# Performance work log

Measured on AMD Instinct MI355X. Metric: run time of the kernel, lower is better.

## Reference

```python
import jax, jax.numpy as jnp
import numpy as np

DIM = 1024
NUM_HEADS = 16
HEAD_DIM = DIM // NUM_HEADS


def setup_inputs() -> dict:
    key = jax.random.key(0)
    ks = jax.random.split(key, 16)
    B, Sx, Sy = 4, 1024, 1024
    s = 1.0 / np.sqrt(DIM)
    inp = {
        'x': jax.random.normal(ks[0], (B, Sx, DIM), dtype=jnp.float32),
        'y': jax.random.normal(ks[1], (B, Sy, DIM), dtype=jnp.float32),
    }
    names = ['Kx', 'Qx', 'Vx', 'Ky', 'Vy', 'out']
    for i, n in enumerate(names):
        inp[f'W_{n}'] = jax.random.uniform(ks[2 + 2 * i], (DIM, DIM), dtype=jnp.float32, minval=-s, maxval=s)
        inp[f'b_{n}'] = jax.random.uniform(ks[3 + 2 * i], (DIM,), dtype=jnp.float32, minval=-s, maxval=s)
    return inp


def _heads(t, B, S):
    # [B, S, DIM] -> [B, H, S, Dh]
    return t.reshape(B, S, NUM_HEADS, HEAD_DIM).transpose(0, 2, 1, 3)


def _attn(x, y, W_Kx, b_Kx, W_Qx, b_Qx, W_Vx, b_Vx, W_Ky, b_Ky, W_Vy, b_Vy, W_out, b_out):
    B, Sx, _ = x.shape
    Sy = y.shape[1]
    lin = lambda t, W, b: t @ W.T + b
    Q = _heads(lin(x, W_Qx, b_Qx), B, Sx)
    Kc = jnp.concatenate([_heads(lin(x, W_Kx, b_Kx), B, Sx), _heads(lin(y, W_Ky, b_Ky), B, Sy)], axis=2)
    Vc = jnp.concatenate([_heads(lin(x, W_Vx, b_Vx), B, Sx), _heads(lin(y, W_Vy, b_Vy), B, Sy)], axis=2)
    scores = jnp.einsum('bhqd,bhkd->bhqk', Q, Kc) / np.sqrt(HEAD_DIM).astype(np.float32)
    w = jax.nn.softmax(scores, axis=-1)
    o = jnp.einsum('bhqk,bhkd->bhqd', w, Vc)  # [B, H, Sx, Dh]
    o = o.transpose(0, 2, 1, 3).reshape(B, Sx, DIM)
    return lin(o, W_out, b_out)


def reference(x, y, W_Kx, b_Kx, W_Qx, b_Qx, W_Vx, b_Vx, W_Ky, b_Ky, W_Vy, b_Vy, W_out, b_out):
    return _attn(x, y, W_Kx, b_Kx, W_Qx, b_Qx, W_Vx, b_Vx, W_Ky, b_Ky, W_Vy, b_Vy, W_out, b_out)
```

## Files before the change

kernel.cpp:

```cpp
#include <hip/hip_runtime.h>

#define DIMN 1024
#define NH 16
#define DH 64
#define SXX 1024
#define SKV 2048

typedef __bf16 bf16x8 __attribute__((ext_vector_type(8)));
typedef float f32x4 __attribute__((ext_vector_type(4)));
typedef unsigned short us8 __attribute__((ext_vector_type(8)));

__device__ __forceinline__ unsigned short f2bs(float f) {
    return (unsigned short)((__builtin_bit_cast(unsigned int, f) + 0x8000u) >> 16);
}
__device__ __forceinline__ unsigned int pk2(float a, float b) {
    return ((__builtin_bit_cast(unsigned int, a) + 0x8000u) >> 16)
         | ((__builtin_bit_cast(unsigned int, b) + 0x8000u) & 0xffff0000u);
}
__device__ __forceinline__ void gl_lds16(const void* g, void* l) {
    __builtin_amdgcn_global_load_lds(
        (const __attribute__((address_space(1))) unsigned int*)g,
        (__attribute__((address_space(3))) unsigned int*)l, 16, 0, 0);
}

struct CvtArgs {
    const float* src[8];
    unsigned short* dst[8];
    int start[8];
};
__global__ __launch_bounds__(256) void cvt_all(CvtArgs a) {
    int b = blockIdx.x;
    int r = 0;
#pragma unroll
    for (int i = 1; i < 8; i++) r += (b >= a.start[i]);
    int off = ((b - a.start[r]) * 256 + (int)threadIdx.x) * 8;
    const float* s = a.src[r] + off;
    float4 f0 = *(const float4*)(s);
    float4 f1 = *(const float4*)(s + 4);
    us8 o;
    o[0] = f2bs(f0.x); o[1] = f2bs(f0.y); o[2] = f2bs(f0.z); o[3] = f2bs(f0.w);
    o[4] = f2bs(f1.x); o[5] = f2bs(f1.y); o[6] = f2bs(f1.z); o[7] = f2bs(f1.w);
    *(us8*)(a.dst[r] + off) = o;
}

__device__ __forceinline__ void gemm_core(const unsigned short* __restrict__ A,
                                          const unsigned short* __restrict__ W,
                                          unsigned short* As, unsigned short* Bs,
                                          int m0, int n0, f32x4 (&acc)[4][4]) {
    const int K = DIMN;
    int tid = threadIdx.x, wave = tid >> 6, lane = tid & 63;
    int l15 = lane & 15, quad = lane >> 4;
    int wm = wave >> 1, wn = wave & 1;
    int srow = wave * 8 + (lane >> 3);
    int gcol = ((lane & 7) ^ (lane >> 3)) * 8;
    const unsigned short* gA = A + (size_t)(m0 + srow) * K + gcol;
    const unsigned short* gW = W + (size_t)(n0 + srow) * K + gcol;
    int ldsoff = wave * 512;
    int slot0 = (quad ^ (l15 & 7)) * 8;

    auto stage = [&](int buf, int k0) {
        unsigned short* lA = As + buf * 8192 + ldsoff;
        unsigned short* lB = Bs + buf * 8192 + ldsoff;
#pragma unroll
        for (int j = 0; j < 4; j++) {
            gl_lds16(gA + k0 + (size_t)j * 32 * K, lA + j * 2048);
            gl_lds16(gW + k0 + (size_t)j * 32 * K, lB + j * 2048);
        }
    };

    stage(0, 0);
    for (int k0 = 0; k0 < K; k0 += 64) {
        int buf = (k0 >> 6) & 1;
        __syncthreads();
        if (k0 + 64 < K) stage(buf ^ 1, k0 + 64);
        const unsigned short* as = As + buf * 8192;
        const unsigned short* bs = Bs + buf * 8192;
#pragma unroll
        for (int kk = 0; kk < 2; kk++) {
            int sl = slot0 ^ (kk * 32);
            bf16x8 af[4], bf[4];
#pragma unroll
            for (int mi = 0; mi < 4; mi++)
                af[mi] = __builtin_bit_cast(bf16x8, *(const us8*)(&as[(wm * 64 + mi * 16 + l15) * 64 + sl]));
#pragma unroll
            for (int ni = 0; ni < 4; ni++)
                bf[ni] = __builtin_bit_cast(bf16x8, *(const us8*)(&bs[(wn * 64 + ni * 16 + l15) * 64 + sl]));
#pragma unroll
            for (int mi = 0; mi < 4; mi++)
#pragma unroll
                for (int ni = 0; ni < 4; ni++)
                    acc[mi][ni] = __builtin_amdgcn_mfma_f32_16x16x32_bf16(af[mi], bf[ni], acc[mi][ni], 0, 0, 0);
        }
    }
}

__global__ __launch_bounds__(256, 2) void gemm_proj(
        const unsigned short* __restrict__ xb, const unsigned short* __restrict__ yb,
        const unsigned short* __restrict__ Wb,
        const float* __restrict__ b_Kx, const float* __restrict__ b_Qx, const float* __restrict__ b_Ky,
        const float* __restrict__ b_Vx, const float* __restrict__ b_Vy,
        unsigned short* __restrict__ Qd, unsigned short* __restrict__ Kd,
        unsigned short* __restrict__ Vd, float qscale) {
    __shared__ __align__(16) unsigned short As[2 * 128 * 64];
    __shared__ __align__(16) unsigned short Bs[2 * 128 * 64];
    int bx = blockIdx.x;
    int tid = threadIdx.x, wave = tid >> 6, lane = tid & 63;
    int l15 = lane & 15, quad = lane >> 4;
    int wm = wave >> 1, wn = wave & 1;

    f32x4 acc[4][4] = {};

    if (bx < 768) {
        int sub = bx >> 8, t = bx & 255;
        int n0 = (t & 7) * 128, m0 = (t >> 3) * 128;
        const unsigned short* A = (sub == 2) ? yb : xb;
        const unsigned short* W = Wb + (size_t)((sub == 0) ? 0 : (sub == 1) ? 1 : 3) * 1048576;
        const float* bp = (sub == 0) ? b_Kx : (sub == 1) ? b_Qx : b_Ky;
        int roff = (sub == 2) ? 1024 : 0;
        float sc = (sub == 1) ? qscale : 1.0f;

        gemm_core(A, W, As, Bs, m0, n0, acc);

#pragma unroll
        for (int mi = 0; mi < 4; mi++) {
            int mbase = m0 + wm * 64 + mi * 16 + quad * 4;
#pragma unroll
            for (int ni = 0; ni < 4; ni++) {
                int n = n0 + wn * 64 + ni * 16 + l15;
                float bv = bp[n];
                int h = n >> 6, d = n & 63;
#pragma unroll
                for (int r = 0; r < 4; r++) {
                    float v = (acc[mi][ni][r] + bv) * sc;
                    int mm = mbase + r;
                    int bidx = mm >> 10, s = mm & 1023;
                    if (sub == 1)
                        Qd[((size_t)(bidx * NH + h) * SXX + s) * DH + d] = f2bs(v);
                    else
                        Kd[((size_t)(bidx * NH + h) * SKV + s + roff) * DH + d] = f2bs(v);
                }
            }
        }
    } else {
        int u = bx - 768;
        int side = u >> 8, t = u & 255;
        int m0 = (t & 7) * 128, n0 = (t >> 3) * 128;
        const unsigned short* Wv = Wb + (size_t)(side ? 4 : 2) * 1048576;
        const unsigned short* act = side ? yb : xb;
        const float* bp = side ? b_Vy : b_Vx;
        int roff = side ? 1024 : 0;

        gemm_core(Wv, act, As, Bs, m0, n0, acc);

#pragma unroll
        for (int mi = 0; mi < 4; mi++) {
            int mbase = m0 + wm * 64 + mi * 16 + quad * 4;
#pragma unroll
            for (int ni = 0; ni < 4; ni++) {
                int n = n0 + wn * 64 + ni * 16 + l15;
                int bidx = n >> 10, s = n & 1023;
#pragma unroll
                for (int r = 0; r < 4; r++) {
                    int m = mbase + r;
                    int h = m >> 6, d = m & 63;
                    float v = acc[mi][ni][r] + bp[m];
                    Vd[((size_t)(bidx * NH + h) * DH + d) * SKV + s + roff] = f2bs(v);
                }
            }
        }
    }
}

__global__ __launch_bounds__(256, 2) void gemm_out(
        const unsigned short* __restrict__ Ob, const unsigned short* __restrict__ Wo,
        const float* __restrict__ bo, float* __restrict__ outp) {
    __shared__ __align__(16) unsigned short As[2 * 64 * 64];
    __shared__ __align__(16) unsigned short Bs[2 * 128 * 64];
    const int K = DIMN;
    int tid = threadIdx.x, wave = tid >> 6, lane = tid & 63;
    int l15 = lane & 15, quad = lane >> 4;
    int wm = wave >> 1, wn = wave & 1;
    int n0 = blockIdx.x * 128, m0 = blockIdx.y * 64;

    int srow = wave * 8 + (lane >> 3);
    int gcol = ((lane & 7) ^ (lane >> 3)) * 8;
    const unsigned short* gA = Ob + (size_t)(m0 + srow) * K + gcol;
    const unsigned short* gW = Wo + (size_t)(n0 + srow) * K + gcol;
    int ldsoff = wave * 512;
    int slot0 = (quad ^ (l15 & 7)) * 8;

    auto stage = [&](int buf, int k0) {
        unsigned short* lA = As + buf * 4096 + ldsoff;
        unsigned short* lB = Bs + buf * 8192 + ldsoff;
#pragma unroll
        for (int j = 0; j < 2; j++)
            gl_lds16(gA + k0 + (size_t)j * 32 * K, lA + j * 2048);
#pragma unroll
        for (int j = 0; j < 4; j++)
            gl_lds16(gW + k0 + (size_t)j * 32 * K, lB + j * 2048);
    };

    f32x4 acc[2][4] = {};
    stage(0, 0);
    for (int k0 = 0; k0 < K; k0 += 64) {
        int buf = (k0 >> 6) & 1;
        __syncthreads();
        if (k0 + 64 < K) stage(buf ^ 1, k0 + 64);
        const unsigned short* as = As + buf * 4096;
        const unsigned short* bs = Bs + buf * 8192;
#pragma unroll
        for (int kk = 0; kk < 2; kk++) {
            int sl = slot0 ^ (kk * 32);
            bf16x8 af[2], bf[4];
#pragma unroll
            for (int mi = 0; mi < 2; mi++)
                af[mi] = __builtin_bit_cast(bf16x8, *(const us8*)(&as[(wm * 32 + mi * 16 + l15) * 64 + sl]));
#pragma unroll
            for (int ni = 0; ni < 4; ni++)
                bf[ni] = __builtin_bit_cast(bf16x8, *(const us8*)(&bs[(wn * 64 + ni * 16 + l15) * 64 + sl]));
#pragma unroll
            for (int mi = 0; mi < 2; mi++)
#pragma unroll
                for (int ni = 0; ni < 4; ni++)
                    acc[mi][ni] = __builtin_amdgcn_mfma_f32_16x16x32_bf16(af[mi], bf[ni], acc[mi][ni], 0, 0, 0);
        }
    }

#pragma unroll
    for (int mi = 0; mi < 2; mi++) {
        int mbase = m0 + wm * 32 + mi * 16 + quad * 4;
#pragma unroll
        for (int ni = 0; ni < 4; ni++) {
            int n = n0 + wn * 64 + ni * 16 + l15;
            float bv = bo[n];
#pragma unroll
            for (int r = 0; r < 4; r++)
                outp[(size_t)(mbase + r) * DIMN + n] = acc[mi][ni][r] + bv;
        }
    }
}

__global__ __launch_bounds__(256, 2) void flash_attn(
        const unsigned short* __restrict__ Qb,
        const unsigned short* __restrict__ Kc,
        const unsigned short* __restrict__ Vt,
        unsigned short* __restrict__ Ob) {
    __shared__ __align__(16) unsigned short Ks[2][64 * 64];
    __shared__ __align__(16) unsigned short Vs[2][64 * 64];
    __shared__ __align__(16) unsigned short Ps[4][32 * 64];
    int tid = threadIdx.x, wave = tid >> 6, lane = tid & 63;
    int l15 = lane & 15, quad = lane >> 4;
    int bh = blockIdx.x;
    int qbase = blockIdx.y * 128 + wave * 32;

    const unsigned short* Qp = Qb + ((size_t)bh * SXX + qbase) * DH;
    bf16x8 bq[2][2];
#pragma unroll
    for (int qt = 0; qt < 2; qt++) {
        bq[qt][0] = __builtin_bit_cast(bf16x8, *(const us8*)(&Qp[(qt * 16 + l15) * DH + quad * 8]));
        bq[qt][1] = __builtin_bit_cast(bf16x8, *(const us8*)(&Qp[(qt * 16 + l15) * DH + 32 + quad * 8]));
    }

    const unsigned short* Kg = Kc + (size_t)bh * SKV * DH;
    const unsigned short* Vg = Vt + (size_t)bh * DH * SKV;

    int srow_lo = 8 * wave + (lane >> 3);
    int srow_hi = srow_lo + 32;
    int swz = ((lane & 7) ^ (lane >> 3)) * 8;
    int sl = (lane & 7) * 8;

    us8 pk0, pk1, pv0, pv1;
    auto gload = [&](int c) {
        pk0 = *(const us8*)(Kg + (size_t)(c + srow_lo) * DH + swz);
        pk1 = *(const us8*)(Kg + (size_t)(c + srow_hi) * DH + swz);
        pv0 = *(const us8*)(Vg + (size_t)srow_lo * SKV + c + swz);
        pv1 = *(const us8*)(Vg + (size_t)srow_hi * SKV + c + swz);
    };
    auto lstore = [&](int buf) {
        *(us8*)(&Ks[buf][srow_lo * 64 + sl]) = pk0;
        *(us8*)(&Ks[buf][srow_hi * 64 + sl]) = pk1;
        *(us8*)(&Vs[buf][srow_lo * 64 + sl]) = pv0;
        *(us8*)(&Vs[buf][srow_hi * 64 + sl]) = pv1;
    };

    f32x4 o[2][4] = {};
    float lsum[2] = {0.f, 0.f};
    int cA = (quad ^ (l15 & 7)) * 8;

    gload(0);
    lstore(0);
    __syncthreads();

    for (int c = 0; c < SKV; c += 64) {
        int cur = (c >> 6) & 1;
        bool more = (c + 64) < SKV;
        if (more) gload(c + 64);

        const unsigned short* ks = &Ks[cur][0];
        bf16x8 ak0[4], ak1[4];
#pragma unroll
        for (int ni = 0; ni < 4; ni++) {
            int row = (ni * 16 + l15) * 64;
            ak0[ni] = __builtin_bit_cast(bf16x8, *(const us8*)(ks + row + cA));
            ak1[ni] = __builtin_bit_cast(bf16x8, *(const us8*)(ks + row + (cA ^ 32)));
        }

        unsigned short* pw = &Ps[wave][0];
#pragma unroll
        for (int qt = 0; qt < 2; qt++) {
#pragma unroll
            for (int ni = 0; ni < 4; ni++) {
                f32x4 z = {};
                z = __builtin_amdgcn_mfma_f32_16x16x32_bf16(ak0[ni], bq[qt][0], z, 0, 0, 0);
                z = __builtin_amdgcn_mfma_f32_16x16x32_bf16(ak1[ni], bq[qt][1], z, 0, 0, 0);
                float p0 = __builtin_amdgcn_exp2f(z[0]);
                float p1 = __builtin_amdgcn_exp2f(z[1]);
                float p2 = __builtin_amdgcn_exp2f(z[2]);
                float p3 = __builtin_amdgcn_exp2f(z[3]);
                lsum[qt] += (p0 + p1) + (p2 + p3);
                unsigned int lo = pk2(p0, p1);
                unsigned int hi = pk2(p2, p3);
                int c8p = (2 * ni + (quad >> 1)) ^ (l15 & 7);
                *(uint2*)(pw + (qt * 16 + l15) * 64 + c8p * 8 + (quad & 1) * 4) = make_uint2(lo, hi);
            }
        }

        const unsigned short* vs = &Vs[cur][0];
        bf16x8 av0[4], av1[4];
#pragma unroll
        for (int ni = 0; ni < 4; ni++) {
            int row = (ni * 16 + l15) * 64;
            av0[ni] = __builtin_bit_cast(bf16x8, *(const us8*)(vs + row + cA));
            av1[ni] = __builtin_bit_cast(bf16x8, *(const us8*)(vs + row + (cA ^ 32)));
        }
#pragma unroll
        for (int qt = 0; qt < 2; qt++) {
            bf16x8 ap0 = __builtin_bit_cast(bf16x8, *(const us8*)(pw + (qt * 16 + l15) * 64 + cA));
            bf16x8 ap1 = __builtin_bit_cast(bf16x8, *(const us8*)(pw + (qt * 16 + l15) * 64 + (cA ^ 32)));
#pragma unroll
            for (int ni = 0; ni < 4; ni++) {
                o[qt][ni] = __builtin_amdgcn_mfma_f32_16x16x32_bf16(ap0, av0[ni], o[qt][ni], 0, 0, 0);
                o[qt][ni] = __builtin_amdgcn_mfma_f32_16x16x32_bf16(ap1, av1[ni], o[qt][ni], 0, 0, 0);
            }
        }

        if (more) lstore(1 - cur);
        __syncthreads();
    }

    int b = bh >> 4, h = bh & 15;
#pragma unroll
    for (int qt = 0; qt < 2; qt++) {
        float ls = lsum[qt];
        ls += __shfl_xor(ls, 16);
        ls += __shfl_xor(ls, 32);
#pragma unroll
        for (int r = 0; r < 4; r++) {
            float lt = __shfl(ls, quad * 4 + r);
            float inv = __builtin_amdgcn_rcpf(lt);
            int q = qbase + qt * 16 + quad * 4 + r;
#pragma unroll
            for (int ni = 0; ni < 4; ni++)
                Ob[((size_t)b * SXX + q) * DIMN + h * DH + ni * 16 + l15] = f2bs(o[qt][ni][r] * inv);
        }
    }
}

extern "C" void kernel_launch(void* const* d_in, const int* in_sizes, int n_in,
                              void* d_out, int out_size, void* d_ws, size_t ws_size,
                              hipStream_t stream) {
    (void)in_sizes; (void)n_in; (void)out_size; (void)ws_size;
    const float* x     = (const float*)d_in[0];
    const float* y     = (const float*)d_in[1];
    const float* W_Kx  = (const float*)d_in[2];
    const float* b_Kx  = (const float*)d_in[3];
    const float* W_Qx  = (const float*)d_in[4];
    const float* b_Qx  = (const float*)d_in[5];
    const float* W_Vx  = (const float*)d_in[6];
    const float* b_Vx  = (const float*)d_in[7];
    const float* W_Ky  = (const float*)d_in[8];
    const float* b_Ky  = (const float*)d_in[9];
    const float* W_Vy  = (const float*)d_in[10];
    const float* b_Vy  = (const float*)d_in[11];
    const float* W_out = (const float*)d_in[12];
    const float* b_out = (const float*)d_in[13];
    float* out = (float*)d_out;

    char* ws = (char*)d_ws;
    unsigned short* xb  = (unsigned short*)(ws);
    unsigned short* yb  = (unsigned short*)(ws + (size_t)( 8 << 20));
    unsigned short* Qb  = (unsigned short*)(ws + (size_t)(16 << 20));
    unsigned short* Kcw = (unsigned short*)(ws + (size_t)(24 << 20));
    unsigned short* Vtw = (unsigned short*)(ws + (size_t)(40 << 20));
    unsigned short* Obw = (unsigned short*)(ws + (size_t)(56 << 20));
    unsigned short* Wb  = (unsigned short*)(ws + (size_t)(64 << 20));

    CvtArgs ca;
    ca.src[0] = x;     ca.dst[0] = xb;                 ca.start[0] = 0;
    ca.src[1] = y;     ca.dst[1] = yb;                 ca.start[1] = 2048;
    ca.src[2] = W_Kx;  ca.dst[2] = Wb + 0u * 1048576;  ca.start[2] = 4096;
    ca.src[3] = W_Qx;  ca.dst[3] = Wb + 1u * 1048576;  ca.start[3] = 4608;
    ca.src[4] = W_Vx;  ca.dst[4] = Wb + 2u * 1048576;  ca.start[4] = 5120;
    ca.src[5] = W_Ky;  ca.dst[5] = Wb + 3u * 1048576;  ca.start[5] = 5632;
    ca.src[6] = W_Vy;  ca.dst[6] = Wb + 4u * 1048576;  ca.start[6] = 6144;
    ca.src[7] = W_out; ca.dst[7] = Wb + 5u * 1048576;  ca.start[7] = 6656;
    cvt_all<<<7168, 256, 0, stream>>>(ca);

    const float qscale = 0.125f * 1.44269504088896340736f;
    gemm_proj<<<1280, 256, 0, stream>>>(xb, yb, Wb, b_Kx, b_Qx, b_Ky, b_Vx, b_Vy,
                                        Qb, Kcw, Vtw, qscale);
    flash_attn<<<dim3(64, 8), 256, 0, stream>>>(Qb, Kcw, Vtw, Obw);
    gemm_out<<<dim3(8, 64), 256, 0, stream>>>(Obw, Wb + 5u * 1048576, b_out, out);
}
```

Before: 246.2 us.

## Replace direct global-to-LDS double buffering with register-staged single-buffer GEMM loads

Both projection and output GEMMs stop using global_load_lds into a double-buffered LDS tile. They now prefetch the next K-slice into registers, then write it to a single LDS buffer after a barrier. This halves LDS usage, which could allow more resident blocks. In exchange it adds a second barrier per iteration and extra VGPRs and LDS write instructions, so loads and MFMA work may overlap less.

New measurement: 236.0 us. 4.1% less time.

```diff
diff --git a/kernel.cpp b/kernel.cpp
--- a/kernel.cpp
+++ b/kernel.cpp
@@ -16,11 +16,6 @@
 __device__ __forceinline__ unsigned int pk2(float a, float b) {
     return ((__builtin_bit_cast(unsigned int, a) + 0x8000u) >> 16)
          | ((__builtin_bit_cast(unsigned int, b) + 0x8000u) & 0xffff0000u);
-}
-__device__ __forceinline__ void gl_lds16(const void* g, void* l) {
-    __builtin_amdgcn_global_load_lds(
-        (const __attribute__((address_space(1))) unsigned int*)g,
-        (__attribute__((address_space(3))) unsigned int*)l, 16, 0, 0);
 }
 
 struct CvtArgs {
@@ -55,36 +50,41 @@
     int gcol = ((lane & 7) ^ (lane >> 3)) * 8;
     const unsigned short* gA = A + (size_t)(m0 + srow) * K + gcol;
     const unsigned short* gW = W + (size_t)(n0 + srow) * K + gcol;
-    int ldsoff = wave * 512;
+    int ldswr = wave * 512 + lane * 8;
     int slot0 = (quad ^ (l15 & 7)) * 8;
 
-    auto stage = [&](int buf, int k0) {
-        unsigned short* lA = As + buf * 8192 + ldsoff;
-        unsigned short* lB = Bs + buf * 8192 + ldsoff;
+    us8 pa[4], pw[4];
+    auto gload = [&](int k0) {
 #pragma unroll
         for (int j = 0; j < 4; j++) {
-            gl_lds16(gA + k0 + (size_t)j * 32 * K, lA + j * 2048);
-            gl_lds16(gW + k0 + (size_t)j * 32 * K, lB + j * 2048);
-        }
-    };
-
-    stage(0, 0);
+            pa[j] = *(const us8*)(gA + k0 + (size_t)j * 32 * K);
+            pw[j] = *(const us8*)(gW + k0 + (size_t)j * 32 * K);
+        }
+    };
+    auto lwrite = [&]() {
+#pragma unroll
+        for (int j = 0; j < 4; j++) {
+            *(us8*)(&As[ldswr + j * 2048]) = pa[j];
+            *(us8*)(&Bs[ldswr + j * 2048]) = pw[j];
+        }
+    };
+
+    gload(0);
     for (int k0 = 0; k0 < K; k0 += 64) {
-        int buf = (k0 >> 6) & 1;
+        if (k0) __syncthreads();
+        lwrite();
+        if (k0 + 64 < K) gload(k0 + 64);
         __syncthreads();
-        if (k0 + 64 < K) stage(buf ^ 1, k0 + 64);
-        const unsigned short* as = As + buf * 8192;
-        const unsigned short* bs = Bs + buf * 8192;
 #pragma unroll
         for (int kk = 0; kk < 2; kk++) {
             int sl = slot0 ^ (kk * 32);
             bf16x8 af[4], bf[4];
 #pragma unroll
             for (int mi = 0; mi < 4; mi++)
-                af[mi] = __builtin_bit_cast(bf16x8, *(const us8*)(&as[(wm * 64 + mi * 16 + l15) * 64 + sl]));
+                af[mi] = __builtin_bit_cast(bf16x8, *(const us8*)(&As[(wm * 64 + mi * 16 + l15) * 64 + sl]));
 #pragma unroll
             for (int ni = 0; ni < 4; ni++)
-                bf[ni] = __builtin_bit_cast(bf16x8, *(const us8*)(&bs[(wn * 64 + ni * 16 + l15) * 64 + sl]));
+                bf[ni] = __builtin_bit_cast(bf16x8, *(const us8*)(&Bs[(wn * 64 + ni * 16 + l15) * 64 + sl]));
 #pragma unroll
             for (int mi = 0; mi < 4; mi++)
 #pragma unroll
@@ -101,8 +101,8 @@
         const float* __restrict__ b_Vx, const float* __restrict__ b_Vy,
         unsigned short* __restrict__ Qd, unsigned short* __restrict__ Kd,
         unsigned short* __restrict__ Vd, float qscale) {
-    __shared__ __align__(16) unsigned short As[2 * 128 * 64];
-    __shared__ __align__(16) unsigned short Bs[2 * 128 * 64];
+    __shared__ __align__(16) unsigned short As[128 * 64];
+    __shared__ __align__(16) unsigned short Bs[128 * 64];
     int bx = blockIdx.x;
     int tid = threadIdx.x, wave = tid >> 6, lane = tid & 63;
     int l15 = lane & 15, quad = lane >> 4;
@@ -174,8 +174,8 @@
 __global__ __launch_bounds__(256, 2) void gemm_out(
         const unsigned short* __restrict__ Ob, const unsigned short* __restrict__ Wo,
         const float* __restrict__ bo, float* __restrict__ outp) {
-    __shared__ __align__(16) unsigned short As[2 * 64 * 64];
-    __shared__ __align__(16) unsigned short Bs[2 * 128 * 64];
+    __shared__ __align__(16) unsigned short As[64 * 64];
+    __shared__ __align__(16) unsigned short Bs[128 * 64];
     const int K = DIMN;
     int tid = threadIdx.x, wave = tid >> 6, lane = tid & 63;
     int l15 = lane & 15, quad = lane >> 4;
@@ -186,38 +186,44 @@
     int gcol = ((lane & 7) ^ (lane >> 3)) * 8;
     const unsigned short* gA = Ob + (size_t)(m0 + srow) * K + gcol;
     const unsigned short* gW = Wo + (size_t)(n0 + srow) * K + gcol;
-    int ldsoff = wave * 512;
+    int ldswr = wave * 512 + lane * 8;
     int slot0 = (quad ^ (l15 & 7)) * 8;
 
-    auto stage = [&](int buf, int k0) {
-        unsigned short* lA = As + buf * 4096 + ldsoff;
-        unsigned short* lB = Bs + buf * 8192 + ldsoff;
+    us8 pa[2], pw[4];
+    auto gload = [&](int k0) {
 #pragma unroll
         for (int j = 0; j < 2; j++)
-            gl_lds16(gA + k0 + (size_t)j * 32 * K, lA + j * 2048);
+            pa[j] = *(const us8*)(gA + k0 + (size_t)j * 32 * K);
 #pragma unroll
         for (int j = 0; j < 4; j++)
-            gl_lds16(gW + k0 + (size_t)j * 32 * K, lB + j * 2048);
+            pw[j] = *(const us8*)(gW + k0 + (size_t)j * 32 * K);
+    };
+    auto lwrite = [&]() {
+#pragma unroll
+        for (int j = 0; j < 2; j++)
+            *(us8*)(&As[ldswr + j * 2048]) = pa[j];
+#pragma unroll
+        for (int j = 0; j < 4; j++)
+            *(us8*)(&Bs[ldswr + j * 2048]) = pw[j];
     };
 
     f32x4 acc[2][4] = {};
-    stage(0, 0);
+    gload(0);
     for (int k0 = 0; k0 < K; k0 += 64) {
-        int buf = (k0 >> 6) & 1;
+        if (k0) __syncthreads();
+        lwrite();
+        if (k0 + 64 < K) gload(k0 + 64);
         __syncthreads();
-        if (k0 + 64 < K) stage(buf ^ 1, k0 + 64);
-        const unsigned short* as = As + buf * 4096;
-        const unsigned short* bs = Bs + buf * 8192;
 #pragma unroll
         for (int kk = 0; kk < 2; kk++) {
             int sl = slot0 ^ (kk * 32);
             bf16x8 af[2], bf[4];
 #pragma unroll
             for (int mi = 0; mi < 2; mi++)
-                af[mi] = __builtin_bit_cast(bf16x8, *(const us8*)(&as[(wm * 32 + mi * 16 + l15) * 64 + sl]));
+                af[mi] = __builtin_bit_cast(bf16x8, *(const us8*)(&As[(wm * 32 + mi * 16 + l15) * 64 + sl]));
 #pragma unroll
             for (int ni = 0; ni < 4; ni++)
-                bf[ni] = __builtin_bit_cast(bf16x8, *(const us8*)(&bs[(wn * 64 + ni * 16 + l15) * 64 + sl]));
+                bf[ni] = __builtin_bit_cast(bf16x8, *(const us8*)(&Bs[(wn * 64 + ni * 16 + l15) * 64 + sl]));
 #pragma unroll
             for (int mi = 0; mi < 2; mi++)
 #pragma unroll
```
